# Kernel optimization log

Hardware: AMD Instinct MI355X
Metric: run time of the kernel (lower is better)

## Reference

```python
import jax, jax.numpy as jnp
import numpy as np

NEG = -1e8

def _leaky_relu(x):
    return jnp.where(x >= 0, x, 0.2 * x)

def setup_inputs() -> dict:
    key = jax.random.key(0)
    k1, k2, k3, k4, k5 = jax.random.split(key, 5)
    n, dn, de = 1024, 128, 128
    node = jax.random.normal(k1, (n, dn), dtype=jnp.float32)
    group = jnp.zeros((n,), dtype=jnp.int32)  # SpectralClustering(n_clusters=1) -> all zeros
    W_emb = jax.random.normal(k2, (de, dn), dtype=jnp.float32) * (1.0 / np.sqrt(dn))
    b_emb = jax.random.normal(k3, (de,), dtype=jnp.float32) * 0.01
    w_att = jax.random.normal(k4, (2 * de,), dtype=jnp.float32) * (1.0 / np.sqrt(2 * de))
    b_att = jax.random.normal(k5, (1,), dtype=jnp.float32) * 0.01
    return {"node": node, "group": group, "W_emb": W_emb, "b_emb": b_emb,
            "w_att": w_att, "b_att": b_att}

def reference(node, group, W_emb, b_emb, w_att, b_att):
    # node: [n, dn]; edge scorer decomposes into rank-1 sum since the
    # attention Linear acts on cat([emb(node_j), emb(node_i)]).
    de = W_emb.shape[0]
    E = node @ W_emb.T + b_emb                      # [n, de]
    s_other = E @ w_att[:de]                        # contribution of node_j (column)
    s_self = E @ w_att[de:]                         # contribution of node_i (row)
    edge = s_self[:, None] + s_other[None, :] + b_att[0]   # [n, n]

    same = group[:, None] == group[None, :]         # self_flag == group_ext
    pos_mask = jnp.where(same, 1.0, NEG)
    neg_mask = jnp.where(same, NEG, 1.0)

    # softmax over dim=0 (rows, per column), matching nn.Softmax(dim=0)
    pos_alpha = jax.nn.softmax(_leaky_relu(edge * pos_mask), axis=0)
    neg_alpha = jax.nn.softmax(_leaky_relu(edge * neg_mask), axis=0)

    # pos_feature[i,j,:] = relu(pos_alpha[i,j] * node[j]); sum over j
    feat = jax.nn.relu(pos_alpha[:, :, None] * node) + jax.nn.relu(neg_alpha[:, :, None] * node)
    return jnp.sum(feat, axis=1)                    # [n, dn]
```

## Files before the change

### kernel.cpp

```cpp
#include <hip/hip_runtime.h>
#include <hip/hip_bf16.h>

#define NEGC (-1e8f)

__device__ __forceinline__ float lrelu(float x) { return x >= 0.f ? x : 0.2f * x; }

__device__ __forceinline__ void edge_pq(float ss, float soj, bool same,
                                        float& p, float& q) {
    float e = ss + soj;
    float pin = same ? e : e * NEGC;
    float nin = same ? e * NEGC : e;
    p = lrelu(pin);
    q = lrelu(nin);
}

__global__ __launch_bounds__(128) void k1_prep_score(
        const float* __restrict__ node,
        const float* __restrict__ W_emb,
        const float* __restrict__ b_emb,
        const float* __restrict__ w_att,
        float* __restrict__ s_other,
        float* __restrict__ s_self) {
    int lane = threadIdx.x;
    float a1 = 0.f, a2 = 0.f;
    for (int e = 0; e < 128; ++e) {
        float w = W_emb[e * 128 + lane];
        a1 += w * w_att[e];
        a2 += w * w_att[128 + e];
    }
    __shared__ float u1[128], u2[128];
    u1[lane] = a1;
    u2[lane] = a2;

    float c1 = b_emb[lane] * w_att[lane];
    float c2 = b_emb[lane] * w_att[128 + lane];
#pragma unroll
    for (int off = 32; off > 0; off >>= 1) {
        c1 += __shfl_xor(c1, off, 64);
        c2 += __shfl_xor(c2, off, 64);
    }
    __shared__ float cw[4];
    if ((lane & 63) == 0) { cw[(lane >> 6) * 2] = c1; cw[(lane >> 6) * 2 + 1] = c2; }
    __syncthreads();
    c1 = cw[0] + cw[2];
    c2 = cw[1] + cw[3];

    int i = blockIdx.x * 128 + lane;
    const float4* row4 = (const float4*)(node + (size_t)i * 128);
    const float4* u14 = (const float4*)u1;
    const float4* u24 = (const float4*)u2;
    float b1 = 0.f, b2 = 0.f;
#pragma unroll 8
    for (int k = 0; k < 32; ++k) {
        float4 x = row4[k];
        float4 v1 = u14[k];
        float4 v2 = u24[k];
        b1 += x.x * v1.x + x.y * v1.y + x.z * v1.z + x.w * v1.w;
        b2 += x.x * v2.x + x.y * v2.y + x.z * v2.z + x.w * v2.w;
    }
    s_other[i] = b1 + c1;
    s_self[i]  = b2 + c2;
}

__global__ __launch_bounds__(256) void k2_col_stats(
        const float* __restrict__ s_self,
        const float* __restrict__ s_other,
        const int* __restrict__ group,
        const float* __restrict__ b_att,
        float* __restrict__ cmp, float* __restrict__ icsp,
        float* __restrict__ cmn, float* __restrict__ icsn) {
    int j = blockIdx.x * 4 + (threadIdx.x >> 6);
    int lane = threadIdx.x & 63;
    float soj = s_other[j] + b_att[0];
    int gj = group[j];

    float pv[16], nv[16];
    float pmax = -3.4e38f, nmax = -3.4e38f;
#pragma unroll
    for (int k = 0; k < 16; ++k) {
        int i = lane + k * 64;
        float p, q;
        edge_pq(s_self[i], soj, group[i] == gj, p, q);
        pv[k] = p; nv[k] = q;
        pmax = fmaxf(pmax, p);
        nmax = fmaxf(nmax, q);
    }
#pragma unroll
    for (int off = 32; off > 0; off >>= 1) {
        pmax = fmaxf(pmax, __shfl_xor(pmax, off, 64));
        nmax = fmaxf(nmax, __shfl_xor(nmax, off, 64));
    }
    float psum = 0.f, nsum = 0.f;
#pragma unroll
    for (int k = 0; k < 16; ++k) {
        psum += __expf(pv[k] - pmax);
        nsum += __expf(nv[k] - nmax);
    }
#pragma unroll
    for (int off = 32; off > 0; off >>= 1) {
        psum += __shfl_xor(psum, off, 64);
        nsum += __shfl_xor(nsum, off, 64);
    }
    if (lane == 0) {
        cmp[j] = pmax; icsp[j] = 1.f / psum;
        cmn[j] = nmax; icsn[j] = 1.f / nsum;
    }
}

#define BI 4
__global__ __launch_bounds__(512) void k3_out(
        const float* __restrict__ node,
        const float* __restrict__ s_self,
        const float* __restrict__ s_other,
        const int* __restrict__ group,
        const float* __restrict__ b_att,
        const float* __restrict__ cmp, const float* __restrict__ icsp,
        const float* __restrict__ cmn, const float* __restrict__ icsn,
        float* __restrict__ out) {
    int t = threadIdx.x;
    int i0 = blockIdx.x * BI;

    __shared__ float buf[8192];
    __shared__ float ss_l[BI];
    __shared__ int   g_l[BI];
    if (t < BI) { ss_l[t] = s_self[i0 + t]; g_l[t] = group[i0 + t]; }
    __syncthreads();

    float ba = b_att[0];
#pragma unroll
    for (int e = 0; e < 8; ++e) {
        int idx = t + e * 512;
        int r = idx >> 10;
        int j = idx & 1023;
        float soj = s_other[j] + ba;
        float p, q;
        edge_pq(ss_l[r], soj, group[j] == g_l[r], p, q);
        buf[r * 1024 + j] = __expf(p - cmp[j]) * icsp[j]
                          + __expf(q - cmn[j]) * icsn[j];
    }
    __syncthreads();

    int lane = t & 31;
    int g = t >> 5;
    const float4* nf4 = (const float4*)node;

    float4 acc[BI];
#pragma unroll
    for (int r = 0; r < BI; ++r) acc[r] = make_float4(0.f, 0.f, 0.f, 0.f);

#pragma unroll 8
    for (int j = g; j < 1024; j += 16) {
        float4 x = nf4[(size_t)j * 32 + lane];
        float4 rn;
        rn.x = fmaxf(x.x, 0.f); rn.y = fmaxf(x.y, 0.f);
        rn.z = fmaxf(x.z, 0.f); rn.w = fmaxf(x.w, 0.f);
#pragma unroll
        for (int r = 0; r < BI; ++r) {
            float a = buf[r * 1024 + j];
            acc[r].x += a * rn.x; acc[r].y += a * rn.y;
            acc[r].z += a * rn.z; acc[r].w += a * rn.w;
        }
    }

    __syncthreads();
    float4* red = (float4*)buf;
#pragma unroll
    for (int r = 0; r < BI; ++r) red[g * 128 + r * 32 + lane] = acc[r];
    __syncthreads();

    int r = t >> 7;
    int d = t & 127;
    float sum = 0.f;
#pragma unroll
    for (int gg = 0; gg < 16; ++gg)
        sum += buf[gg * 512 + r * 128 + d];
    out[(size_t)(i0 + r) * 128 + d] = sum;
}

extern "C" void kernel_launch(void* const* d_in, const int* in_sizes, int n_in,
                              void* d_out, int out_size, void* d_ws, size_t ws_size,
                              hipStream_t stream) {
    const float* node  = (const float*)d_in[0];
    const int*   group = (const int*)d_in[1];
    const float* W_emb = (const float*)d_in[2];
    const float* b_emb = (const float*)d_in[3];
    const float* w_att = (const float*)d_in[4];
    const float* b_att = (const float*)d_in[5];
    float* out = (float*)d_out;

    const int n = in_sizes[1];

    float* w = (float*)d_ws;
    float* s_other = w;
    float* s_self  = w + n;
    float* cmp     = w + 2 * n;
    float* icsp    = w + 3 * n;
    float* cmn     = w + 4 * n;
    float* icsn    = w + 5 * n;

    k1_prep_score<<<n / 128, 128, 0, stream>>>(node, W_emb, b_emb, w_att,
                                               s_other, s_self);
    k2_col_stats<<<n / 4, 256, 0, stream>>>(s_self, s_other, group, b_att,
                                            cmp, icsp, cmn, icsn);
    k3_out<<<n / BI, 512, 0, stream>>>(node, s_self, s_other, group, b_att,
                                       cmp, icsp, cmn, icsn, out);
}
```

Before: 25.24 us.

## Fuse three kernels into one persistent kernel with grid barriers

Replaces the three separate launches (score prep, column softmax stats, output accumulation) with a single 128-block kernel that uses atomic-counter grid barriers between phases. This removes two kernel launch gaps. Each block now handles 8 output rows instead of 4, and the probability tile is stored interleaved so one pair of float4 LDS reads serves all rows. The reduction now uses a cross-half shuffle before the LDS pass. The risks are spin-wait overhead, a reliance on all 128 blocks being co-resident, an extra memset per call, and hardcoded n=1024.

```diff
diff --git a/kernel.cpp b/kernel.cpp
--- a/kernel.cpp
+++ b/kernel.cpp
@@ -2,6 +2,9 @@
 #include <hip/hip_bf16.h>
 
 #define NEGC (-1e8f)
+#define NBLK 128
+#define NTHR 512
+#define BI 8
 
 __device__ __forceinline__ float lrelu(float x) { return x >= 0.f ? x : 0.2f * x; }
 
@@ -14,167 +17,193 @@
     q = lrelu(nin);
 }
 
-__global__ __launch_bounds__(128) void k1_prep_score(
-        const float* __restrict__ node,
-        const float* __restrict__ W_emb,
-        const float* __restrict__ b_emb,
-        const float* __restrict__ w_att,
-        float* __restrict__ s_other,
-        float* __restrict__ s_self) {
-    int lane = threadIdx.x;
-    float a1 = 0.f, a2 = 0.f;
-    for (int e = 0; e < 128; ++e) {
-        float w = W_emb[e * 128 + lane];
-        a1 += w * w_att[e];
-        a2 += w * w_att[128 + e];
-    }
-    __shared__ float u1[128], u2[128];
-    u1[lane] = a1;
-    u2[lane] = a2;
-
-    float c1 = b_emb[lane] * w_att[lane];
-    float c2 = b_emb[lane] * w_att[128 + lane];
-#pragma unroll
-    for (int off = 32; off > 0; off >>= 1) {
-        c1 += __shfl_xor(c1, off, 64);
-        c2 += __shfl_xor(c2, off, 64);
-    }
-    __shared__ float cw[4];
-    if ((lane & 63) == 0) { cw[(lane >> 6) * 2] = c1; cw[(lane >> 6) * 2 + 1] = c2; }
+__device__ __forceinline__ void grid_barrier(unsigned* ctr) {
     __syncthreads();
-    c1 = cw[0] + cw[2];
-    c2 = cw[1] + cw[3];
-
-    int i = blockIdx.x * 128 + lane;
-    const float4* row4 = (const float4*)(node + (size_t)i * 128);
-    const float4* u14 = (const float4*)u1;
-    const float4* u24 = (const float4*)u2;
-    float b1 = 0.f, b2 = 0.f;
+    if (threadIdx.x == 0) {
+        __threadfence();
+        __hip_atomic_fetch_add(ctr, 1u, __ATOMIC_ACQ_REL, __HIP_MEMORY_SCOPE_AGENT);
+        while (__hip_atomic_load(ctr, __ATOMIC_RELAXED, __HIP_MEMORY_SCOPE_AGENT)
+               < (unsigned)NBLK) {
+            __builtin_amdgcn_s_sleep(2);
+        }
+        __threadfence();
+    }
+    __syncthreads();
+}
+
+__global__ __launch_bounds__(NTHR) void fused_kernel(
+        const float* __restrict__ node, const int* __restrict__ group,
+        const float* __restrict__ W_emb, const float* __restrict__ b_emb,
+        const float* __restrict__ w_att, const float* __restrict__ b_att,
+        float* __restrict__ s_other_g, float* __restrict__ s_self_g,
+        float* __restrict__ cmp_g, float* __restrict__ icsp_g,
+        float* __restrict__ cmn_g, float* __restrict__ icsn_g,
+        unsigned* __restrict__ bar, float* __restrict__ out) {
+    int t = threadIdx.x;
+    int b = blockIdx.x;
+    int wv = t >> 6, lane = t & 63;
+    float ba = b_att[0];
+
+    __shared__ float lds[8192];
+
+    {
+        int k = t & 127, q = t >> 7;
+        float p1 = 0.f, p2 = 0.f;
+        for (int e = 32 * q; e < 32 * q + 32; ++e) {
+            float w = W_emb[e * 128 + k];
+            p1 += w * w_att[e];
+            p2 += w * w_att[128 + e];
+        }
+        lds[q * 256 + k] = p1;
+        lds[q * 256 + 128 + k] = p2;
+        __syncthreads();
+        if (t < 128) {
+            lds[1024 + t] = lds[t] + lds[256 + t] + lds[512 + t] + lds[768 + t];
+        } else if (t < 256) {
+            int kk = t - 128;
+            lds[1152 + kk] = lds[128 + kk] + lds[384 + kk] + lds[640 + kk] + lds[896 + kk];
+        } else if (t < 320) {
+            int l = t - 256;
+            float cc = b_emb[l] * w_att[l] + b_emb[64 + l] * w_att[64 + l];
+            for (int off = 32; off > 0; off >>= 1) cc += __shfl_xor(cc, off, 64);
+            if (l == 0) lds[1280] = cc;
+        } else if (t < 384) {
+            int l = t - 320;
+            float cc = b_emb[l] * w_att[128 + l] + b_emb[64 + l] * w_att[192 + l];
+            for (int off = 32; off > 0; off >>= 1) cc += __shfl_xor(cc, off, 64);
+            if (l == 0) lds[1281] = cc;
+        }
+        __syncthreads();
+        int i = b * BI + wv;
+        const float2* row2 = (const float2*)(node + (size_t)i * 128);
+        const float2* u12 = (const float2*)&lds[1024];
+        const float2* u22 = (const float2*)&lds[1152];
+        float2 x = row2[lane];
+        float2 ua = u12[lane];
+        float2 ub = u22[lane];
+        float d1 = x.x * ua.x + x.y * ua.y;
+        float d2 = x.x * ub.x + x.y * ub.y;
+        for (int off = 32; off > 0; off >>= 1) {
+            d1 += __shfl_xor(d1, off, 64);
+            d2 += __shfl_xor(d2, off, 64);
+        }
+        if (lane == 0) {
+            s_other_g[i] = d1 + lds[1280];
+            s_self_g[i]  = d2 + lds[1281];
+        }
+    }
+    grid_barrier(bar + 0);
+
+    {
+        int j = b * BI + wv;
+        float soj = s_other_g[j] + ba;
+        int gj = group[j];
+        float pv[16], nv[16];
+        float pmax = -3.4e38f, nmax = -3.4e38f;
+#pragma unroll
+        for (int k = 0; k < 16; ++k) {
+            int i = lane + k * 64;
+            float p, q;
+            edge_pq(s_self_g[i], soj, group[i] == gj, p, q);
+            pv[k] = p; nv[k] = q;
+            pmax = fmaxf(pmax, p);
+            nmax = fmaxf(nmax, q);
+        }
+#pragma unroll
+        for (int off = 32; off > 0; off >>= 1) {
+            pmax = fmaxf(pmax, __shfl_xor(pmax, off, 64));
+            nmax = fmaxf(nmax, __shfl_xor(nmax, off, 64));
+        }
+        float ps = 0.f, ns = 0.f;
+#pragma unroll
+        for (int k = 0; k < 16; ++k) {
+            ps += __expf(pv[k] - pmax);
+            ns += __expf(nv[k] - nmax);
+        }
+#pragma unroll
+        for (int off = 32; off > 0; off >>= 1) {
+            ps += __shfl_xor(ps, off, 64);
+            ns += __shfl_xor(ns, off, 64);
+        }
+        if (lane == 0) {
+            cmp_g[j] = pmax; icsp_g[j] = 1.f / ps;
+            cmn_g[j] = nmax; icsn_g[j] = 1.f / ns;
+        }
+    }
+    grid_barrier(bar + 1);
+
+    {
+        int i0 = b * BI;
+        float ss[BI]; int gl[BI];
+#pragma unroll
+        for (int r = 0; r < BI; ++r) { ss[r] = s_self_g[i0 + r]; gl[r] = group[i0 + r]; }
+
+#pragma unroll
+        for (int e = 0; e < 2; ++e) {
+            int j = t + e * 512;
+            float soj = s_other_g[j] + ba;
+            int gj = group[j];
+            float mp = cmp_g[j], ip = icsp_g[j], mn = cmn_g[j], iq = icsn_g[j];
+            float tmp[8];
+#pragma unroll
+            for (int r = 0; r < BI; ++r) {
+                float p, q;
+                edge_pq(ss[r], soj, gj == gl[r], p, q);
+                tmp[r] = __expf(p - mp) * ip + __expf(q - mn) * iq;
+            }
+            *(float4*)&lds[j * 8]     = make_float4(tmp[0], tmp[1], tmp[2], tmp[3]);
+            *(float4*)&lds[j * 8 + 4] = make_float4(tmp[4], tmp[5], tmp[6], tmp[7]);
+        }
+        __syncthreads();
+
+        int g = t >> 5, l32 = t & 31;
+        const float4* nf4 = (const float4*)node;
+        float4 acc[BI];
+#pragma unroll
+        for (int r = 0; r < BI; ++r) acc[r] = make_float4(0.f, 0.f, 0.f, 0.f);
+
 #pragma unroll 8
-    for (int k = 0; k < 32; ++k) {
-        float4 x = row4[k];
-        float4 v1 = u14[k];
-        float4 v2 = u24[k];
-        b1 += x.x * v1.x + x.y * v1.y + x.z * v1.z + x.w * v1.w;
-        b2 += x.x * v2.x + x.y * v2.y + x.z * v2.z + x.w * v2.w;
-    }
-    s_other[i] = b1 + c1;
-    s_self[i]  = b2 + c2;
-}
-
-__global__ __launch_bounds__(256) void k2_col_stats(
-        const float* __restrict__ s_self,
-        const float* __restrict__ s_other,
-        const int* __restrict__ group,
-        const float* __restrict__ b_att,
-        float* __restrict__ cmp, float* __restrict__ icsp,
-        float* __restrict__ cmn, float* __restrict__ icsn) {
-    int j = blockIdx.x * 4 + (threadIdx.x >> 6);
-    int lane = threadIdx.x & 63;
-    float soj = s_other[j] + b_att[0];
-    int gj = group[j];
-
-    float pv[16], nv[16];
-    float pmax = -3.4e38f, nmax = -3.4e38f;
-#pragma unroll
-    for (int k = 0; k < 16; ++k) {
-        int i = lane + k * 64;
-        float p, q;
-        edge_pq(s_self[i], soj, group[i] == gj, p, q);
-        pv[k] = p; nv[k] = q;
-        pmax = fmaxf(pmax, p);
-        nmax = fmaxf(nmax, q);
-    }
-#pragma unroll
-    for (int off = 32; off > 0; off >>= 1) {
-        pmax = fmaxf(pmax, __shfl_xor(pmax, off, 64));
-        nmax = fmaxf(nmax, __shfl_xor(nmax, off, 64));
-    }
-    float psum = 0.f, nsum = 0.f;
-#pragma unroll
-    for (int k = 0; k < 16; ++k) {
-        psum += __expf(pv[k] - pmax);
-        nsum += __expf(nv[k] - nmax);
-    }
-#pragma unroll
-    for (int off = 32; off > 0; off >>= 1) {
-        psum += __shfl_xor(psum, off, 64);
-        nsum += __shfl_xor(nsum, off, 64);
-    }
-    if (lane == 0) {
-        cmp[j] = pmax; icsp[j] = 1.f / psum;
-        cmn[j] = nmax; icsn[j] = 1.f / nsum;
-    }
-}
-
-#define BI 4
-__global__ __launch_bounds__(512) void k3_out(
-        const float* __restrict__ node,
-        const float* __restrict__ s_self,
-        const float* __restrict__ s_other,
-        const int* __restrict__ group,
-        const float* __restrict__ b_att,
-        const float* __restrict__ cmp, const float* __restrict__ icsp,
-        const float* __restrict__ cmn, const float* __restrict__ icsn,
-        float* __restrict__ out) {
-    int t = threadIdx.x;
-    int i0 = blockIdx.x * BI;
-
-    __shared__ float buf[8192];
-    __shared__ float ss_l[BI];
-    __shared__ int   g_l[BI];
-    if (t < BI) { ss_l[t] = s_self[i0 + t]; g_l[t] = group[i0 + t]; }
-    __syncthreads();
-
-    float ba = b_att[0];
-#pragma unroll
-    for (int e = 0; e < 8; ++e) {
-        int idx = t + e * 512;
-        int r = idx >> 10;
-        int j = idx & 1023;
-        float soj = s_other[j] + ba;
-        float p, q;
-        edge_pq(ss_l[r], soj, group[j] == g_l[r], p, q);
-        buf[r * 1024 + j] = __expf(p - cmp[j]) * icsp[j]
-                          + __expf(q - cmn[j]) * icsn[j];
-    }
-    __syncthreads();
-
-    int lane = t & 31;
-    int g = t >> 5;
-    const float4* nf4 = (const float4*)node;
-
-    float4 acc[BI];
-#pragma unroll
-    for (int r = 0; r < BI; ++r) acc[r] = make_float4(0.f, 0.f, 0.f, 0.f);
-
-#pragma unroll 8
-    for (int j = g; j < 1024; j += 16) {
-        float4 x = nf4[(size_t)j * 32 + lane];
-        float4 rn;
-        rn.x = fmaxf(x.x, 0.f); rn.y = fmaxf(x.y, 0.f);
-        rn.z = fmaxf(x.z, 0.f); rn.w = fmaxf(x.w, 0.f);
+        for (int j = g; j < 1024; j += 16) {
+            float4 a0 = *(const float4*)&lds[j * 8];
+            float4 a1 = *(const float4*)&lds[j * 8 + 4];
+            float4 x = nf4[(size_t)j * 32 + l32];
+            float4 rn = make_float4(fmaxf(x.x, 0.f), fmaxf(x.y, 0.f),
+                                    fmaxf(x.z, 0.f), fmaxf(x.w, 0.f));
+            float aa[8] = {a0.x, a0.y, a0.z, a0.w, a1.x, a1.y, a1.z, a1.w};
+#pragma unroll
+            for (int r = 0; r < BI; ++r) {
+                acc[r].x += aa[r] * rn.x; acc[r].y += aa[r] * rn.y;
+                acc[r].z += aa[r] * rn.z; acc[r].w += aa[r] * rn.w;
+            }
+        }
+
 #pragma unroll
         for (int r = 0; r < BI; ++r) {
-            float a = buf[r * 1024 + j];
-            acc[r].x += a * rn.x; acc[r].y += a * rn.y;
-            acc[r].z += a * rn.z; acc[r].w += a * rn.w;
-        }
-    }
-
-    __syncthreads();
-    float4* red = (float4*)buf;
-#pragma unroll
-    for (int r = 0; r < BI; ++r) red[g * 128 + r * 32 + lane] = acc[r];
-    __syncthreads();
-
-    int r = t >> 7;
-    int d = t & 127;
-    float sum = 0.f;
-#pragma unroll
-    for (int gg = 0; gg < 16; ++gg)
-        sum += buf[gg * 512 + r * 128 + d];
-    out[(size_t)(i0 + r) * 128 + d] = sum;
+            acc[r].x += __shfl_xor(acc[r].x, 32, 64);
+            acc[r].y += __shfl_xor(acc[r].y, 32, 64);
+            acc[r].z += __shfl_xor(acc[r].z, 32, 64);
+            acc[r].w += __shfl_xor(acc[r].w, 32, 64);
+        }
+
+        __syncthreads();
+        if ((t & 32) == 0) {
+            int hg = g >> 1;
+            float4* redf4 = (float4*)&lds[0];
+#pragma unroll
+            for (int r = 0; r < BI; ++r) redf4[hg * (BI * 32) + r * 32 + l32] = acc[r];
+        }
+        __syncthreads();
+
+#pragma unroll
+        for (int s = 0; s < 2; ++s) {
+            int o = t + s * 512;
+            int r = o >> 7, d = o & 127;
+            float sum = 0.f;
+#pragma unroll
+            for (int hg = 0; hg < 8; ++hg) sum += lds[hg * 1024 + r * 128 + d];
+            out[(size_t)(i0 + r) * 128 + d] = sum;
+        }
+    }
 }
 
 extern "C" void kernel_launch(void* const* d_in, const int* in_sizes, int n_in,
@@ -188,20 +217,17 @@
     const float* b_att = (const float*)d_in[5];
     float* out = (float*)d_out;
 
-    const int n = in_sizes[1];
-
     float* w = (float*)d_ws;
     float* s_other = w;
-    float* s_self  = w + n;
-    float* cmp     = w + 2 * n;
-    float* icsp    = w + 3 * n;
-    float* cmn     = w + 4 * n;
-    float* icsn    = w + 5 * n;
-
-    k1_prep_score<<<n / 128, 128, 0, stream>>>(node, W_emb, b_emb, w_att,
-                                               s_other, s_self);
-    k2_col_stats<<<n / 4, 256, 0, stream>>>(s_self, s_other, group, b_att,
-                                            cmp, icsp, cmn, icsn);
-    k3_out<<<n / BI, 512, 0, stream>>>(node, s_self, s_other, group, b_att,
-                                       cmp, icsp, cmn, icsn, out);
-}
+    float* s_self  = w + 1024;
+    float* cmp     = w + 2048;
+    float* icsp    = w + 3072;
+    float* cmn     = w + 4096;
+    float* icsn    = w + 5120;
+    unsigned* bar  = (unsigned*)((char*)d_ws + 32768);
+
+    hipMemsetAsync(bar, 0, 8, stream);
+    fused_kernel<<<NBLK, NTHR, 0, stream>>>(node, group, W_emb, b_emb, w_att,
+                                            b_att, s_other, s_self, cmp, icsp,
+                                            cmn, icsn, bar, out);
+}
```

Result: slower. 41.40 us (+64.0%).

## Fuse score computation and column softmax stats into one kernel

Applied to the files above, without the earlier changes.

Merges the score-prep kernel and the column-statistics kernel into a single kernel. Each block redundantly computes the projected weight vectors and all 1024 s_self scores into shared memory, then computes softmax max and sum for its 8 columns. This removes one kernel launch and the global round trip of s_self between kernels. In exchange, every one of the 128 blocks repeats the full W_emb reduction and reads the whole node matrix, and the sizes are now hardcoded to n=1024.

```diff
diff --git a/kernel.cpp b/kernel.cpp
--- a/kernel.cpp
+++ b/kernel.cpp
@@ -14,73 +14,97 @@
     q = lrelu(nin);
 }
 
-__global__ __launch_bounds__(128) void k1_prep_score(
-        const float* __restrict__ node,
-        const float* __restrict__ W_emb,
-        const float* __restrict__ b_emb,
-        const float* __restrict__ w_att,
-        float* __restrict__ s_other,
-        float* __restrict__ s_self) {
-    int lane = threadIdx.x;
-    float a1 = 0.f, a2 = 0.f;
-    for (int e = 0; e < 128; ++e) {
-        float w = W_emb[e * 128 + lane];
-        a1 += w * w_att[e];
-        a2 += w * w_att[128 + e];
-    }
+__global__ __launch_bounds__(512) void kA_scores_stats(
+        const float* __restrict__ node, const int* __restrict__ group,
+        const float* __restrict__ W_emb, const float* __restrict__ b_emb,
+        const float* __restrict__ w_att, const float* __restrict__ b_att,
+        float* __restrict__ s_other_g, float* __restrict__ s_self_g,
+        float* __restrict__ cmp_g, float* __restrict__ icsp_g,
+        float* __restrict__ cmn_g, float* __restrict__ icsn_g) {
+    int t = threadIdx.x;
+    int b = blockIdx.x;
+    int wv = t >> 6, lane = t & 63;
+
+    __shared__ float part[1024];
     __shared__ float u1[128], u2[128];
-    u1[lane] = a1;
-    u2[lane] = a2;
-
-    float c1 = b_emb[lane] * w_att[lane];
-    float c2 = b_emb[lane] * w_att[128 + lane];
-#pragma unroll
-    for (int off = 32; off > 0; off >>= 1) {
-        c1 += __shfl_xor(c1, off, 64);
-        c2 += __shfl_xor(c2, off, 64);
-    }
-    __shared__ float cw[4];
-    if ((lane & 63) == 0) { cw[(lane >> 6) * 2] = c1; cw[(lane >> 6) * 2 + 1] = c2; }
-    __syncthreads();
-    c1 = cw[0] + cw[2];
-    c2 = cw[1] + cw[3];
-
-    int i = blockIdx.x * 128 + lane;
-    const float4* row4 = (const float4*)(node + (size_t)i * 128);
-    const float4* u14 = (const float4*)u1;
+    __shared__ float sself[1024];
+    __shared__ int   grp[1024];
+    __shared__ float cc[2];
+    __shared__ float sothr[8];
+
+    {
+        int k = t & 127, q = t >> 7;
+        float p1 = 0.f, p2 = 0.f;
+        for (int e = 32 * q; e < 32 * q + 32; ++e) {
+            float w = W_emb[e * 128 + k];
+            p1 += w * w_att[e];
+            p2 += w * w_att[128 + e];
+        }
+        part[q * 256 + k] = p1;
+        part[q * 256 + 128 + k] = p2;
+    }
+    __syncthreads();
+    if (t < 128) {
+        u1[t] = part[t] + part[256 + t] + part[512 + t] + part[768 + t];
+    } else if (t < 256) {
+        int k = t - 128;
+        u2[k] = part[128 + k] + part[384 + k] + part[640 + k] + part[896 + k];
+    } else if (t < 320) {
+        int l = t - 256;
+        float c = b_emb[l] * w_att[l] + b_emb[64 + l] * w_att[64 + l];
+        for (int off = 32; off > 0; off >>= 1) c += __shfl_xor(c, off, 64);
+        if (l == 0) cc[0] = c;
+    } else if (t < 384) {
+        int l = t - 320;
+        float c = b_emb[l] * w_att[128 + l] + b_emb[64 + l] * w_att[192 + l];
+        for (int off = 32; off > 0; off >>= 1) c += __shfl_xor(c, off, 64);
+        if (l == 0) cc[1] = c;
+    }
+    __syncthreads();
+
     const float4* u24 = (const float4*)u2;
-    float b1 = 0.f, b2 = 0.f;
+#pragma unroll
+    for (int e = 0; e < 2; ++e) {
+        int i = t + e * 512;
+        const float4* row4 = (const float4*)(node + (size_t)i * 128);
+        float a = 0.f;
 #pragma unroll 8
-    for (int k = 0; k < 32; ++k) {
-        float4 x = row4[k];
-        float4 v1 = u14[k];
-        float4 v2 = u24[k];
-        b1 += x.x * v1.x + x.y * v1.y + x.z * v1.z + x.w * v1.w;
-        b2 += x.x * v2.x + x.y * v2.y + x.z * v2.z + x.w * v2.w;
-    }
-    s_other[i] = b1 + c1;
-    s_self[i]  = b2 + c2;
-}
-
-__global__ __launch_bounds__(256) void k2_col_stats(
-        const float* __restrict__ s_self,
-        const float* __restrict__ s_other,
-        const int* __restrict__ group,
-        const float* __restrict__ b_att,
-        float* __restrict__ cmp, float* __restrict__ icsp,
-        float* __restrict__ cmn, float* __restrict__ icsn) {
-    int j = blockIdx.x * 4 + (threadIdx.x >> 6);
-    int lane = threadIdx.x & 63;
-    float soj = s_other[j] + b_att[0];
-    int gj = group[j];
-
+        for (int k = 0; k < 32; ++k) {
+            float4 x = row4[k];
+            float4 v = u24[k];
+            a += x.x * v.x + x.y * v.y + x.z * v.z + x.w * v.w;
+        }
+        sself[i] = a + cc[1];
+        grp[i] = group[i];
+    }
+
+    {
+        int j = b * 8 + wv;
+        const float2* row2 = (const float2*)(node + (size_t)j * 128);
+        const float2* u12 = (const float2*)u1;
+        float2 x = row2[lane], v = u12[lane];
+        float d = x.x * v.x + x.y * v.y;
+        for (int off = 32; off > 0; off >>= 1) d += __shfl_xor(d, off, 64);
+        if (lane == 0) {
+            float so = d + cc[0];
+            sothr[wv] = so;
+            s_other_g[j] = so;
+        }
+    }
+    __syncthreads();
+
+    if (t < 8) s_self_g[b * 8 + t] = sself[b * 8 + t];
+
+    float ba = b_att[0];
+    float soj = sothr[wv] + ba;
+    int gj = grp[b * 8 + wv];
     float pv[16], nv[16];
     float pmax = -3.4e38f, nmax = -3.4e38f;
 #pragma unroll
     for (int k = 0; k < 16; ++k) {
         int i = lane + k * 64;
         float p, q;
-        edge_pq(s_self[i], soj, group[i] == gj, p, q);
+        edge_pq(sself[i], soj, grp[i] == gj, p, q);
         pv[k] = p; nv[k] = q;
         pmax = fmaxf(pmax, p);
         nmax = fmaxf(nmax, q);
@@ -90,25 +114,26 @@
         pmax = fmaxf(pmax, __shfl_xor(pmax, off, 64));
         nmax = fmaxf(nmax, __shfl_xor(nmax, off, 64));
     }
-    float psum = 0.f, nsum = 0.f;
+    float ps = 0.f, ns = 0.f;
 #pragma unroll
     for (int k = 0; k < 16; ++k) {
-        psum += __expf(pv[k] - pmax);
-        nsum += __expf(nv[k] - nmax);
+        ps += __expf(pv[k] - pmax);
+        ns += __expf(nv[k] - nmax);
     }
 #pragma unroll
     for (int off = 32; off > 0; off >>= 1) {
-        psum += __shfl_xor(psum, off, 64);
-        nsum += __shfl_xor(nsum, off, 64);
+        ps += __shfl_xor(ps, off, 64);
+        ns += __shfl_xor(ns, off, 64);
     }
     if (lane == 0) {
-        cmp[j] = pmax; icsp[j] = 1.f / psum;
-        cmn[j] = nmax; icsn[j] = 1.f / nsum;
+        int j = b * 8 + wv;
+        cmp_g[j] = pmax; icsp_g[j] = 1.f / ps;
+        cmn_g[j] = nmax; icsn_g[j] = 1.f / ns;
     }
 }
 
 #define BI 4
-__global__ __launch_bounds__(512) void k3_out(
+__global__ __launch_bounds__(512) void kB_out(
         const float* __restrict__ node,
         const float* __restrict__ s_self,
         const float* __restrict__ s_other,
@@ -188,20 +213,17 @@
     const float* b_att = (const float*)d_in[5];
     float* out = (float*)d_out;
 
-    const int n = in_sizes[1];
-
     float* w = (float*)d_ws;
     float* s_other = w;
-    float* s_self  = w + n;
-    float* cmp     = w + 2 * n;
-    float* icsp    = w + 3 * n;
-    float* cmn     = w + 4 * n;
-    float* icsn    = w + 5 * n;
-
-    k1_prep_score<<<n / 128, 128, 0, stream>>>(node, W_emb, b_emb, w_att,
-                                               s_other, s_self);
-    k2_col_stats<<<n / 4, 256, 0, stream>>>(s_self, s_other, group, b_att,
-                                            cmp, icsp, cmn, icsn);
-    k3_out<<<n / BI, 512, 0, stream>>>(node, s_self, s_other, group, b_att,
-                                       cmp, icsp, cmn, icsn, out);
-}
+    float* s_self  = w + 1024;
+    float* cmp     = w + 2048;
+    float* icsp    = w + 3072;
+    float* cmn     = w + 4096;
+    float* icsn    = w + 5120;
+
+    kA_scores_stats<<<128, 512, 0, stream>>>(node, group, W_emb, b_emb, w_att,
+                                             b_att, s_other, s_self, cmp, icsp,
+                                             cmn, icsn);
+    kB_out<<<256, 512, 0, stream>>>(node, s_self, s_other, group, b_att,
+                                    cmp, icsp, cmn, icsn, out);
+}
```

New measurement: 34.92 us. +38.3%, slower.
